# Kernel tuning notes

Hardware: AMD Instinct MI355X
Metric: run time of the kernel (lower is better)

The kernel has to match this reference:

```python
import jax, jax.numpy as jnp
import numpy as np

T, E, K, H, I = 512, 16, 4, 2880, 2880
G_H, G_I = H // 32, I // 32  # MXFP4 groups of 32 values (16 bytes/block)
ALPHA, LIMIT, EPS = 1.702, 7.0, 1e-5

FP4_VALUES = jnp.array([0.0, 0.5, 1.0, 1.5, 2.0, 3.0, 4.0, 6.0,
                        -0.0, -0.5, -1.0, -1.5, -2.0, -3.0, -4.0, -6.0], jnp.float32)


def dequant_mxfp4(blocks, scales):
    # blocks: uint8 [..., G, 16]; scales: uint8 [..., G] (biased exponent)
    pre = blocks.shape[:-2]
    G, B = blocks.shape[-2], blocks.shape[-1]
    lo = FP4_VALUES[(blocks & 0xF).astype(jnp.int32)]   # [..., G, B]
    hi = FP4_VALUES[(blocks >> 4).astype(jnp.int32)]    # [..., G, B]
    vals = jnp.stack([lo, hi], axis=-1).reshape(*pre, G, B * 2)  # interleave lo/hi per byte
    vals = jnp.ldexp(vals, (scales.astype(jnp.int32) - 127)[..., None])
    return vals.reshape(*pre, G * B * 2)


def swiglu(h):
    g = jnp.minimum(h[..., 0::2], LIMIT)
    l = jnp.clip(h[..., 1::2], -LIMIT, LIMIT)
    return g * jax.nn.sigmoid(ALPHA * g) * (l + 1.0)


def setup_inputs() -> dict:
    key = jax.random.key(0)
    ks = jax.random.split(key, 10)
    x = jax.random.normal(ks[0], (T, H), jnp.float32)
    norm_scale = jnp.ones((H,), jnp.float32)
    gate_w = jax.random.normal(ks[1], (E, H), jnp.float32) * 0.02
    gate_b = jnp.zeros((E,), jnp.float32)
    mlp1_blocks = jax.random.randint(ks[2], (E, 2 * I, G_H, 16), 0, 256, dtype=jnp.uint8)
    mlp1_scales = jax.random.randint(ks[3], (E, 2 * I, G_H), 118, 128, dtype=jnp.uint8)
    mlp1_bias = jax.random.normal(ks[4], (E, 2 * I), jnp.float32) * 0.02
    mlp2_blocks = jax.random.randint(ks[5], (E, H, G_I, 16), 0, 256, dtype=jnp.uint8)
    mlp2_scales = jax.random.randint(ks[6], (E, H, G_I), 118, 128, dtype=jnp.uint8)
    mlp2_bias = jax.random.normal(ks[7], (E, H), jnp.float32) * 0.02
    return {"x": x, "norm_scale": norm_scale, "gate_w": gate_w, "gate_b": gate_b,
            "mlp1_blocks": mlp1_blocks, "mlp1_scales": mlp1_scales, "mlp1_bias": mlp1_bias,
            "mlp2_blocks": mlp2_blocks, "mlp2_scales": mlp2_scales, "mlp2_bias": mlp2_bias}


def reference(x, norm_scale, gate_w, gate_b, mlp1_blocks, mlp1_scales, mlp1_bias,
              mlp2_blocks, mlp2_scales, mlp2_bias):
    # RMSNorm
    t = x * jax.lax.rsqrt(jnp.mean(x * x, axis=-1, keepdims=True) + EPS) * norm_scale
    # router: top-k + softmax over selected logits
    g = t @ gate_w.T + gate_b                      # [T, E]
    vals, idx = jax.lax.top_k(g, K)                # sorted, distinct indices
    w = jax.nn.softmax(vals, axis=-1)              # [T, K]
    n_tok = t.shape[0]
    route = jnp.zeros((n_tok, gate_w.shape[0]), t.dtype)
    route = route.at[jnp.arange(n_tok)[:, None], idx].set(w)  # [T, E] sparse weights
    # expert MLPs (dense dispatch; unrouted experts get zero weight)
    W1 = dequant_mxfp4(mlp1_blocks, mlp1_scales)   # [E, 2I, H]
    h = jnp.einsum('th,ech->tec', t, W1) + mlp1_bias[None]   # [T, E, 2I]
    h = swiglu(h)                                            # [T, E, I]
    W2 = dequant_mxfp4(mlp2_blocks, mlp2_scales)   # [E, H, I]
    o = jnp.einsum('tec,ehc->teh', h, W2) + mlp2_bias[None]  # [T, E, H]
    return x + jnp.einsum('teh,te->th', o, route)
```

## Files before the change

### kernel.cpp

```cpp
#include <hip/hip_runtime.h>
#include <hip/hip_bf16.h>

typedef __attribute__((ext_vector_type(8))) short short8;
typedef __attribute__((ext_vector_type(4))) float f32x4;
typedef __attribute__((ext_vector_type(4))) int i32x4;
typedef __attribute__((ext_vector_type(2))) int i32x2;
typedef __attribute__((ext_vector_type(4))) unsigned u32x4;

#define NTOK 512
#define NEXP 16
#define TOPK 4
#define HD   2880
#define ID   2880
#define N1   5760
#define NGRP 90
#define NKT  45
#define ROWB 5760

__device__ __forceinline__ unsigned perm(unsigned hi, unsigned lo, unsigned sel) {
  return __builtin_amdgcn_perm(hi, lo, sel);
}

__device__ __forceinline__ u32x4 dq_word4(unsigned p, unsigned hbl, unsigned hbh,
                                          unsigned lbl, unsigned lbh) {
  unsigned ph = p >> 4;
  unsigned il = p  & 0x07070707u, sl = p  & 0x08080808u;
  unsigned ih = ph & 0x07070707u, sh = ph & 0x08080808u;
  unsigned hbL = perm(hbh, hbl, il) | (sl << 4);
  unsigned lbL = perm(lbh, lbl, il);
  unsigned hbH = perm(hbh, hbl, ih) | (sh << 4);
  unsigned lbH = perm(lbh, lbl, ih);
  unsigned mL01 = perm(hbL, lbL, 0x05010400u);
  unsigned mL23 = perm(hbL, lbL, 0x07030602u);
  unsigned mH01 = perm(hbH, lbH, 0x05010400u);
  unsigned mH23 = perm(hbH, lbH, 0x07030602u);
  u32x4 w;
  w.x = perm(mH01, mL01, 0x05040100u);
  w.y = perm(mH01, mL01, 0x07060302u);
  w.z = perm(mH23, mL23, 0x05040100u);
  w.w = perm(mH23, mL23, 0x07060302u);
  return w;
}

__device__ __forceinline__ short8 dq_frag(i32x4 q, int sc) {
  unsigned m7 = (unsigned)((127 - sc) << 7);
  unsigned mm = m7 | (m7 << 16);
  unsigned e10 = (0x3F00u - m7) << 16;
  unsigned e32 = 0x3FC03F80u - mm;
  unsigned e54 = 0x40404000u - mm;
  unsigned e76 = 0x40C04080u - mm;
  unsigned hbl = perm(e32, e10, 0x07050301u);
  unsigned hbh = perm(e76, e54, 0x07050301u);
  unsigned lbl = perm(e32, e10, 0x06040200u);
  unsigned lbh = perm(e76, e54, 0x06040200u);
  unsigned pk = (unsigned)q.x | ((unsigned)q.y << 8) |
                ((unsigned)q.z << 16) | ((unsigned)q.w << 24);
  u32x4 w = dq_word4(pk, hbl, hbh, lbl, lbh);
  return __builtin_bit_cast(short8, w);
}

__global__ __launch_bounds__(256)
void rmsnorm_k(const float* __restrict__ x, const float* __restrict__ nsc,
               float* __restrict__ tf, __hip_bfloat16* __restrict__ tb,
               int* __restrict__ cnt)
{
  int t = blockIdx.x;
  if (t == 0 && threadIdx.x < NEXP) cnt[threadIdx.x] = 0;
  const float* xr = x + (size_t)t * HD;
  float s = 0.f;
  for (int i = threadIdx.x; i < HD; i += 256) { float v = xr[i]; s += v * v; }
#pragma unroll
  for (int o = 32; o > 0; o >>= 1) s += __shfl_down(s, o);
  __shared__ float red[4];
  if ((threadIdx.x & 63) == 0) red[threadIdx.x >> 6] = s;
  __syncthreads();
  float tot = red[0] + red[1] + red[2] + red[3];
  float rinv = rsqrtf(tot / (float)HD + 1e-5f);
  for (int i = threadIdx.x; i < HD; i += 256) {
    float v = xr[i] * rinv * nsc[i];
    tf[(size_t)t * HD + i] = v;
    tb[(size_t)t * HD + i] = __float2bfloat16(v);
  }
}

__global__ __launch_bounds__(256)
void router_k(const float* __restrict__ tf, const float* __restrict__ gw,
              const float* __restrict__ gb, float* __restrict__ wpair,
              int* __restrict__ cnt, int* __restrict__ tok_list, int* __restrict__ pair_list)
{
  int t = blockIdx.x;
  int tid = threadIdx.x;
  int e = tid >> 4, l16 = tid & 15;
  const float* tr = tf + (size_t)t * HD;
  float s = 0.f;
  for (int i = l16; i < HD; i += 16) s += tr[i] * gw[e * HD + i];
#pragma unroll
  for (int o = 1; o < 16; o <<= 1) s += __shfl_xor(s, o);
  __shared__ float logits[NEXP];
  if (l16 == 0) logits[e] = s + gb[e];
  __syncthreads();
  if (tid == 0) {
    float v[NEXP];
#pragma unroll
    for (int i = 0; i < NEXP; ++i) v[i] = logits[i];
    int idx[TOPK]; float val[TOPK];
#pragma unroll
    for (int k = 0; k < TOPK; ++k) {
      int bi = 0; float bv = -1e30f;
      for (int i = 0; i < NEXP; ++i) if (v[i] > bv) { bv = v[i]; bi = i; }
      idx[k] = bi; val[k] = bv; v[bi] = -1e30f;
    }
    float mx = val[0], sum = 0.f, w[TOPK];
#pragma unroll
    for (int k = 0; k < TOPK; ++k) { w[k] = __expf(val[k] - mx); sum += w[k]; }
#pragma unroll
    for (int k = 0; k < TOPK; ++k) {
      float wk = w[k] / sum;
      int ee = idx[k];
      int slot = atomicAdd(&cnt[ee], 1);
      tok_list[ee * NTOK + slot]  = t;
      pair_list[ee * NTOK + slot] = t * TOPK + k;
      wpair[t * TOPK + k] = wk;
    }
  }
}

#define SYNC_LGKM do { asm volatile("s_waitcnt lgkmcnt(0)" ::: "memory"); \
    __builtin_amdgcn_sched_barrier(0); __builtin_amdgcn_s_barrier(); \
    __builtin_amdgcn_sched_barrier(0); } while (0)
#define SYNC_PLAIN do { __builtin_amdgcn_sched_barrier(0); __builtin_amdgcn_s_barrier(); \
    __builtin_amdgcn_sched_barrier(0); } while (0)

template<int STAGE, int BN>
__global__ __launch_bounds__(256, 4)
void moe_gemm(const __hip_bfloat16* __restrict__ Asrc,
              const int* __restrict__ Bblk, const int* __restrict__ Bscl,
              const float* __restrict__ Bbias,
              const int* __restrict__ cnt,
              const int* __restrict__ tok_list, const int* __restrict__ pair_list,
              __hip_bfloat16* __restrict__ h_out, float* __restrict__ o_out)
{
  constexpr int NDIM = (STAGE == 1) ? N1 : HD;
  constexpr int NF   = BN / 64;
  const int e  = blockIdx.z;
  const int ne = cnt[e];
  const int m0 = blockIdx.y * 128;
  if (m0 >= ne) return;
  const int n0 = blockIdx.x * BN;
  const int tid = threadIdx.x;
  const int wave = tid >> 6, lane = tid & 63;
  const int l15 = lane & 15, l4 = lane >> 4;

  __shared__ __align__(16) char Abuf[2][16384];

  const int* glist = (STAGE == 1 ? tok_list : pair_list) + e * NTOK;
  const int* plist = pair_list + e * NTOK;

  const char* agp[4];
  int awoff[4];
#pragma unroll
  for (int c = 0; c < 4; ++c) {
    int g    = c * 256 + tid;
    int row  = g >> 3;
    int cb   = (g & 7) * 16;
    int slot = m0 + row; if (slot > ne - 1) slot = ne - 1;
    agp[c]   = (const char*)Asrc + (size_t)glist[slot] * ROWB + cb;
    awoff[c] = row * 128 + (cb ^ ((row & 7) << 4));
  }

  const int wn = wave * (16 * NF);
  unsigned bofs[NF], srow[NF];
#pragma unroll
  for (int f = 0; f < NF; ++f) {
    int row = n0 + wn + f * 16 + l15;
    unsigned rb = (unsigned)(e * NDIM + row) * NGRP;
    bofs[f] = rb * 16 + (unsigned)(l4 * 4);
    srow[f] = rb;
  }

  int aoff[8][2];
#pragma unroll
  for (int mf = 0; mf < 8; ++mf) {
    int row = mf * 16 + l15;
#pragma unroll
    for (int kk = 0; kk < 2; ++kk)
      aoff[mf][kk] = row * 128 + ((kk * 64 + l4 * 16) ^ ((row & 7) << 4));
  }

  f32x4 zero = {0.f, 0.f, 0.f, 0.f};
  f32x4 acc[8][NF];
#pragma unroll
  for (int a = 0; a < 8; ++a)
#pragma unroll
    for (int b = 0; b < NF; ++b) acc[a][b] = zero;

  i32x4 Ar[4];
  i32x4 q[NF][2]; i32x2 sc[NF];
  short8 b[NF][2];

#pragma unroll
  for (int c = 0; c < 4; ++c) Ar[c] = *(const i32x4*)agp[c];
#pragma unroll
  for (int f = 0; f < NF; ++f) {
    q[f][0] = *(const i32x4*)(Bblk + bofs[f]);
    q[f][1] = *(const i32x4*)(Bblk + bofs[f] + 16);
    sc[f]   = *(const i32x2*)(Bscl + srow[f]);
  }
#pragma unroll
  for (int c = 0; c < 4; ++c) *(i32x4*)(Abuf[0] + awoff[c]) = Ar[c];
#pragma unroll
  for (int f = 0; f < NF; ++f) {
    b[f][0] = dq_frag(q[f][0], sc[f].x);
    b[f][1] = dq_frag(q[f][1], sc[f].y);
  }
#pragma unroll
  for (int c = 0; c < 4; ++c) Ar[c] = *(const i32x4*)(agp[c] + 128);
#pragma unroll
  for (int f = 0; f < NF; ++f) {
    q[f][0] = *(const i32x4*)(Bblk + bofs[f] + 2 * 16);
    q[f][1] = *(const i32x4*)(Bblk + bofs[f] + 3 * 16);
    sc[f]   = *(const i32x2*)(Bscl + srow[f] + 2);
  }
  SYNC_LGKM;

  for (int t = 0; t < NKT; ++t) {
    const int cur = t & 1, nxt = cur ^ 1;
    int tld = t + 2; if (tld >= NKT) tld = NKT - 1;

#pragma unroll
    for (int c = 0; c < 4; ++c) *(i32x4*)(Abuf[nxt] + awoff[c]) = Ar[c];
#pragma unroll
    for (int c = 0; c < 4; ++c) Ar[c] = *(const i32x4*)(agp[c] + tld * 128);
    SYNC_LGKM;

    __builtin_amdgcn_s_setprio(1);
#pragma unroll
    for (int kk = 0; kk < 2; ++kk) {
#pragma unroll
      for (int mf = 0; mf < 8; ++mf) {
        short8 af = *(const short8*)(Abuf[cur] + aoff[mf][kk]);
#pragma unroll
        for (int nf = 0; nf < NF; ++nf)
          acc[mf][nf] = __builtin_amdgcn_mfma_f32_16x16x32_bf16(af, b[nf][kk], acc[mf][nf], 0, 0, 0);
      }
    }
    __builtin_amdgcn_s_setprio(0);

#pragma unroll
    for (int f = 0; f < NF; ++f) {
      b[f][0] = dq_frag(q[f][0], sc[f].x);
      b[f][1] = dq_frag(q[f][1], sc[f].y);
    }
#pragma unroll
    for (int f = 0; f < NF; ++f) {
      q[f][0] = *(const i32x4*)(Bblk + bofs[f] + (unsigned)((tld * 2 + 0) * 16));
      q[f][1] = *(const i32x4*)(Bblk + bofs[f] + (unsigned)((tld * 2 + 1) * 16));
      sc[f]   = *(const i32x2*)(Bscl + srow[f] + (unsigned)(tld * 2));
    }
    SYNC_PLAIN;
  }

  if (STAGE == 1) {
#pragma unroll
    for (int ma = 0; ma < 8; ++ma) {
#pragma unroll
      for (int nb = 0; nb < NF; ++nb) {
        int ncol = n0 + wn + nb * 16 + l15;
        float bias = Bbias[e * NDIM + ncol];
#pragma unroll
        for (int j = 0; j < 4; ++j) {
          float u  = acc[ma][nb][j] + bias;
          float up = __shfl_xor(u, 1);
          int slot = m0 + ma * 16 + l4 * 4 + j;
          if (!(lane & 1) && slot < ne) {
            float g  = fminf(u, 7.f);
            float lv = fminf(fmaxf(up, -7.f), 7.f);
            float hv = g / (1.f + __expf(-1.702f * g)) * (lv + 1.f);
            h_out[(size_t)plist[slot] * ID + (ncol >> 1)] = __float2bfloat16(hv);
          }
        }
      }
    }
  } else {
#pragma unroll
    for (int ma = 0; ma < 8; ++ma) {
#pragma unroll
      for (int nb = 0; nb < NF; ++nb) {
        int ncol = n0 + wn + nb * 16 + l15;
        float bias = Bbias[e * NDIM + ncol];
#pragma unroll
        for (int j = 0; j < 4; ++j) {
          int slot = m0 + ma * 16 + l4 * 4 + j;
          if (slot < ne)
            o_out[(size_t)plist[slot] * HD + ncol] = acc[ma][nb][j] + bias;
        }
      }
    }
  }
}

__global__ __launch_bounds__(256)
void final_k(const float* __restrict__ x, const float* __restrict__ obuf,
             const float* __restrict__ wpair, float* __restrict__ out)
{
  int t = blockIdx.x;
  float w0 = wpair[t * 4 + 0], w1 = wpair[t * 4 + 1];
  float w2 = wpair[t * 4 + 2], w3 = wpair[t * 4 + 3];
  const float* o0 = obuf + (size_t)(t * 4) * HD;
  for (int i = threadIdx.x; i < HD; i += 256) {
    float r = x[(size_t)t * HD + i]
            + w0 * o0[i] + w1 * o0[HD + i] + w2 * o0[2 * HD + i] + w3 * o0[3 * HD + i];
    out[(size_t)t * HD + i] = r;
  }
}

extern "C" void kernel_launch(void* const* d_in, const int* in_sizes, int n_in,
                              void* d_out, int out_size, void* d_ws, size_t ws_size,
                              hipStream_t stream)
{
  const float* x    = (const float*)d_in[0];
  const float* nsc  = (const float*)d_in[1];
  const float* gw   = (const float*)d_in[2];
  const float* gb   = (const float*)d_in[3];
  const int*   b1   = (const int*)d_in[4];
  const int*   s1   = (const int*)d_in[5];
  const float* bia1 = (const float*)d_in[6];
  const int*   b2   = (const int*)d_in[7];
  const int*   s2   = (const int*)d_in[8];
  const float* bia2 = (const float*)d_in[9];
  float* out = (float*)d_out;

  char* ws = (char*)d_ws;
  size_t off = 0;
  auto alloc = [&](size_t bytes) {
    char* p = ws + off;
    off = (off + bytes + 255) & ~(size_t)255;
    return p;
  };
  float*           tf    = (float*)alloc((size_t)NTOK * HD * 4);
  __hip_bfloat16*  tb    = (__hip_bfloat16*)alloc((size_t)NTOK * HD * 2);
  __hip_bfloat16*  hbuf  = (__hip_bfloat16*)alloc((size_t)NTOK * TOPK * ID * 2);
  float*           obuf  = (float*)alloc((size_t)NTOK * TOPK * HD * 4);
  float*           wpair = (float*)alloc(NTOK * TOPK * 4);
  int*             cnt   = (int*)alloc(64);
  int*             tokl  = (int*)alloc(NEXP * NTOK * 4);
  int*             pairl = (int*)alloc(NEXP * NTOK * 4);

  rmsnorm_k<<<NTOK, 256, 0, stream>>>(x, nsc, tf, tb, cnt);
  router_k<<<NTOK, 256, 0, stream>>>(tf, gw, gb, wpair, cnt, tokl, pairl);
  moe_gemm<1, 64><<<dim3(N1 / 64, 4, NEXP), 256, 0, stream>>>(tb, b1, s1, bia1, cnt, tokl, pairl, hbuf, nullptr);
  moe_gemm<2, 64><<<dim3(HD / 64, 4, NEXP), 256, 0, stream>>>(hbuf, b2, s2, bia2, cnt, tokl, pairl, nullptr, obuf);
  final_k<<<NTOK, 256, 0, stream>>>(x, obuf, wpair, out);
}
```

Before: 467.6 us.

## Repack int32-per-byte MXFP4 weights and scales into compact bytes before GEMMs

Adds a pack kernel that squeezes the int32-per-byte weight blocks and scales into dense uint8 buffers in workspace on every call. The MoE GEMMs then read 4-byte words instead of 16-byte vectors per fragment, which cuts the bytes the GEMM streams from memory. It also removes the in-kernel byte packing and drops the BN template parameter in favor of a fixed single fragment. The cost is an extra full read of the int32 weights plus a write of the packed copy each call, and a fallback path when the workspace is too small.

```diff
diff --git a/kernel.cpp b/kernel.cpp
--- a/kernel.cpp
+++ b/kernel.cpp
@@ -16,6 +16,11 @@
 #define NGRP 90
 #define NKT  45
 #define ROWB 5760
+
+#define NB1 132710400
+#define NS1 8294400
+#define NB2 66355200
+#define NS2 4147200
 
 __device__ __forceinline__ unsigned perm(unsigned hi, unsigned lo, unsigned sel) {
   return __builtin_amdgcn_perm(hi, lo, sel);
@@ -42,7 +47,7 @@
   return w;
 }
 
-__device__ __forceinline__ short8 dq_frag(i32x4 q, int sc) {
+__device__ __forceinline__ short8 dq_frag(unsigned pk, int sc) {
   unsigned m7 = (unsigned)((127 - sc) << 7);
   unsigned mm = m7 | (m7 << 16);
   unsigned e10 = (0x3F00u - m7) << 16;
@@ -53,10 +58,27 @@
   unsigned hbh = perm(e76, e54, 0x07050301u);
   unsigned lbl = perm(e32, e10, 0x06040200u);
   unsigned lbh = perm(e76, e54, 0x06040200u);
-  unsigned pk = (unsigned)q.x | ((unsigned)q.y << 8) |
-                ((unsigned)q.z << 16) | ((unsigned)q.w << 24);
   u32x4 w = dq_word4(pk, hbl, hbh, lbl, lbh);
   return __builtin_bit_cast(short8, w);
+}
+
+__global__ __launch_bounds__(256)
+void pack_k(const int* __restrict__ in, unsigned char* __restrict__ out, int n16)
+{
+  int i = blockIdx.x * 256 + threadIdx.x;
+  if (i >= n16) return;
+  const i32x4* p = (const i32x4*)(in + (size_t)i * 16);
+  i32x4 a = p[0], b = p[1], c = p[2], d = p[3];
+  u32x4 w;
+  w.x = (unsigned)(a.x & 255) | ((unsigned)(a.y & 255) << 8) |
+        ((unsigned)(a.z & 255) << 16) | ((unsigned)a.w << 24);
+  w.y = (unsigned)(b.x & 255) | ((unsigned)(b.y & 255) << 8) |
+        ((unsigned)(b.z & 255) << 16) | ((unsigned)b.w << 24);
+  w.z = (unsigned)(c.x & 255) | ((unsigned)(c.y & 255) << 8) |
+        ((unsigned)(c.z & 255) << 16) | ((unsigned)c.w << 24);
+  w.w = (unsigned)(d.x & 255) | ((unsigned)(d.y & 255) << 8) |
+        ((unsigned)(d.z & 255) << 16) | ((unsigned)d.w << 24);
+  *(u32x4*)(out + (size_t)i * 16) = w;
 }
 
 __global__ __launch_bounds__(256)
@@ -131,22 +153,22 @@
 #define SYNC_PLAIN do { __builtin_amdgcn_sched_barrier(0); __builtin_amdgcn_s_barrier(); \
     __builtin_amdgcn_sched_barrier(0); } while (0)
 
-template<int STAGE, int BN>
+template<int STAGE, bool PACKED>
 __global__ __launch_bounds__(256, 4)
 void moe_gemm(const __hip_bfloat16* __restrict__ Asrc,
-              const int* __restrict__ Bblk, const int* __restrict__ Bscl,
+              const void* __restrict__ Bblk_, const void* __restrict__ Bscl_,
               const float* __restrict__ Bbias,
               const int* __restrict__ cnt,
               const int* __restrict__ tok_list, const int* __restrict__ pair_list,
               __hip_bfloat16* __restrict__ h_out, float* __restrict__ o_out)
 {
   constexpr int NDIM = (STAGE == 1) ? N1 : HD;
-  constexpr int NF   = BN / 64;
+  constexpr int NF   = 1;
   const int e  = blockIdx.z;
   const int ne = cnt[e];
   const int m0 = blockIdx.y * 128;
   if (m0 >= ne) return;
-  const int n0 = blockIdx.x * BN;
+  const int n0 = blockIdx.x * 64;
   const int tid = threadIdx.x;
   const int wave = tid >> 6, lane = tid & 63;
   const int l15 = lane & 15, l4 = lane >> 4;
@@ -168,15 +190,21 @@
     awoff[c] = row * 128 + (cb ^ ((row & 7) << 4));
   }
 
-  const int wn = wave * (16 * NF);
-  unsigned bofs[NF], srow[NF];
-#pragma unroll
-  for (int f = 0; f < NF; ++f) {
-    int row = n0 + wn + f * 16 + l15;
-    unsigned rb = (unsigned)(e * NDIM + row) * NGRP;
-    bofs[f] = rb * 16 + (unsigned)(l4 * 4);
-    srow[f] = rb;
-  }
+  const int wn = wave * 16;
+  const int brow = n0 + wn + l15;
+  unsigned bofs, srow;
+  if (PACKED) {
+    bofs = (unsigned)(e * NDIM + brow) * (NGRP * 16u) + (unsigned)(l4 * 4);
+    srow = (unsigned)(e * NDIM + brow) * (unsigned)NGRP;
+  } else {
+    unsigned rb = (unsigned)(e * NDIM + brow) * NGRP;
+    bofs = rb * 16 + (unsigned)(l4 * 4);
+    srow = rb;
+  }
+  const unsigned char* Bp = (const unsigned char*)Bblk_;
+  const unsigned char* Sp = (const unsigned char*)Bscl_;
+  const int* Bw = (const int*)Bblk_;
+  const int* Sw = (const int*)Bscl_;
 
   int aoff[8][2];
 #pragma unroll
@@ -190,37 +218,41 @@
   f32x4 zero = {0.f, 0.f, 0.f, 0.f};
   f32x4 acc[8][NF];
 #pragma unroll
-  for (int a = 0; a < 8; ++a)
-#pragma unroll
-    for (int b = 0; b < NF; ++b) acc[a][b] = zero;
+  for (int a = 0; a < 8; ++a) acc[a][0] = zero;
 
   i32x4 Ar[4];
-  i32x4 q[NF][2]; i32x2 sc[NF];
-  short8 b[NF][2];
+  unsigned q0, q1;
+  int scx, scy;
+  short8 b0, b1;
+
+  auto loadB = [&](int tt) {
+    if (PACKED) {
+      q0 = *(const unsigned*)(Bp + bofs + (unsigned)(tt * 32));
+      q1 = *(const unsigned*)(Bp + bofs + (unsigned)(tt * 32 + 16));
+      unsigned sv = *(const unsigned short*)(Sp + srow + (unsigned)(tt * 2));
+      scx = (int)(sv & 255u); scy = (int)(sv >> 8);
+    } else {
+      i32x4 v0 = *(const i32x4*)(Bw + bofs + (unsigned)((tt * 2 + 0) * 16));
+      i32x4 v1 = *(const i32x4*)(Bw + bofs + (unsigned)((tt * 2 + 1) * 16));
+      q0 = (unsigned)(v0.x & 255) | ((unsigned)(v0.y & 255) << 8) |
+           ((unsigned)(v0.z & 255) << 16) | ((unsigned)v0.w << 24);
+      q1 = (unsigned)(v1.x & 255) | ((unsigned)(v1.y & 255) << 8) |
+           ((unsigned)(v1.z & 255) << 16) | ((unsigned)v1.w << 24);
+      i32x2 sv = *(const i32x2*)(Sw + srow + (unsigned)(tt * 2));
+      scx = sv.x; scy = sv.y;
+    }
+  };
 
 #pragma unroll
   for (int c = 0; c < 4; ++c) Ar[c] = *(const i32x4*)agp[c];
-#pragma unroll
-  for (int f = 0; f < NF; ++f) {
-    q[f][0] = *(const i32x4*)(Bblk + bofs[f]);
-    q[f][1] = *(const i32x4*)(Bblk + bofs[f] + 16);
-    sc[f]   = *(const i32x2*)(Bscl + srow[f]);
-  }
+  loadB(0);
 #pragma unroll
   for (int c = 0; c < 4; ++c) *(i32x4*)(Abuf[0] + awoff[c]) = Ar[c];
-#pragma unroll
-  for (int f = 0; f < NF; ++f) {
-    b[f][0] = dq_frag(q[f][0], sc[f].x);
-    b[f][1] = dq_frag(q[f][1], sc[f].y);
-  }
+  b0 = dq_frag(q0, scx);
+  b1 = dq_frag(q1, scy);
 #pragma unroll
   for (int c = 0; c < 4; ++c) Ar[c] = *(const i32x4*)(agp[c] + 128);
-#pragma unroll
-  for (int f = 0; f < NF; ++f) {
-    q[f][0] = *(const i32x4*)(Bblk + bofs[f] + 2 * 16);
-    q[f][1] = *(const i32x4*)(Bblk + bofs[f] + 3 * 16);
-    sc[f]   = *(const i32x2*)(Bscl + srow[f] + 2);
-  }
+  loadB(1);
   SYNC_LGKM;
 
   for (int t = 0; t < NKT; ++t) {
@@ -236,64 +268,49 @@
     __builtin_amdgcn_s_setprio(1);
 #pragma unroll
     for (int kk = 0; kk < 2; ++kk) {
+      short8 bk = kk ? b1 : b0;
 #pragma unroll
       for (int mf = 0; mf < 8; ++mf) {
         short8 af = *(const short8*)(Abuf[cur] + aoff[mf][kk]);
-#pragma unroll
-        for (int nf = 0; nf < NF; ++nf)
-          acc[mf][nf] = __builtin_amdgcn_mfma_f32_16x16x32_bf16(af, b[nf][kk], acc[mf][nf], 0, 0, 0);
+        acc[mf][0] = __builtin_amdgcn_mfma_f32_16x16x32_bf16(af, bk, acc[mf][0], 0, 0, 0);
       }
     }
     __builtin_amdgcn_s_setprio(0);
 
-#pragma unroll
-    for (int f = 0; f < NF; ++f) {
-      b[f][0] = dq_frag(q[f][0], sc[f].x);
-      b[f][1] = dq_frag(q[f][1], sc[f].y);
-    }
-#pragma unroll
-    for (int f = 0; f < NF; ++f) {
-      q[f][0] = *(const i32x4*)(Bblk + bofs[f] + (unsigned)((tld * 2 + 0) * 16));
-      q[f][1] = *(const i32x4*)(Bblk + bofs[f] + (unsigned)((tld * 2 + 1) * 16));
-      sc[f]   = *(const i32x2*)(Bscl + srow[f] + (unsigned)(tld * 2));
-    }
+    b0 = dq_frag(q0, scx);
+    b1 = dq_frag(q1, scy);
+    loadB(tld);
     SYNC_PLAIN;
   }
 
   if (STAGE == 1) {
 #pragma unroll
     for (int ma = 0; ma < 8; ++ma) {
-#pragma unroll
-      for (int nb = 0; nb < NF; ++nb) {
-        int ncol = n0 + wn + nb * 16 + l15;
-        float bias = Bbias[e * NDIM + ncol];
-#pragma unroll
-        for (int j = 0; j < 4; ++j) {
-          float u  = acc[ma][nb][j] + bias;
-          float up = __shfl_xor(u, 1);
-          int slot = m0 + ma * 16 + l4 * 4 + j;
-          if (!(lane & 1) && slot < ne) {
-            float g  = fminf(u, 7.f);
-            float lv = fminf(fmaxf(up, -7.f), 7.f);
-            float hv = g / (1.f + __expf(-1.702f * g)) * (lv + 1.f);
-            h_out[(size_t)plist[slot] * ID + (ncol >> 1)] = __float2bfloat16(hv);
-          }
+      int ncol = n0 + wn + l15;
+      float bias = Bbias[e * NDIM + ncol];
+#pragma unroll
+      for (int j = 0; j < 4; ++j) {
+        float u  = acc[ma][0][j] + bias;
+        float up = __shfl_xor(u, 1);
+        int slot = m0 + ma * 16 + l4 * 4 + j;
+        if (!(lane & 1) && slot < ne) {
+          float g  = fminf(u, 7.f);
+          float lv = fminf(fmaxf(up, -7.f), 7.f);
+          float hv = g / (1.f + __expf(-1.702f * g)) * (lv + 1.f);
+          h_out[(size_t)plist[slot] * ID + (ncol >> 1)] = __float2bfloat16(hv);
         }
       }
     }
   } else {
 #pragma unroll
     for (int ma = 0; ma < 8; ++ma) {
-#pragma unroll
-      for (int nb = 0; nb < NF; ++nb) {
-        int ncol = n0 + wn + nb * 16 + l15;
-        float bias = Bbias[e * NDIM + ncol];
-#pragma unroll
-        for (int j = 0; j < 4; ++j) {
-          int slot = m0 + ma * 16 + l4 * 4 + j;
-          if (slot < ne)
-            o_out[(size_t)plist[slot] * HD + ncol] = acc[ma][nb][j] + bias;
-        }
+      int ncol = n0 + wn + l15;
+      float bias = Bbias[e * NDIM + ncol];
+#pragma unroll
+      for (int j = 0; j < 4; ++j) {
+        int slot = m0 + ma * 16 + l4 * 4 + j;
+        if (slot < ne)
+          o_out[(size_t)plist[slot] * HD + ncol] = acc[ma][0][j] + bias;
       }
     }
   }
@@ -345,10 +362,28 @@
   int*             cnt   = (int*)alloc(64);
   int*             tokl  = (int*)alloc(NEXP * NTOK * 4);
   int*             pairl = (int*)alloc(NEXP * NTOK * 4);
+  unsigned char*   pb1   = (unsigned char*)alloc(NB1);
+  unsigned char*   ps1   = (unsigned char*)alloc(NS1);
+  unsigned char*   pb2   = (unsigned char*)alloc(NB2);
+  unsigned char*   ps2   = (unsigned char*)alloc(NS2);
+  const bool packed = (off <= ws_size);
 
   rmsnorm_k<<<NTOK, 256, 0, stream>>>(x, nsc, tf, tb, cnt);
   router_k<<<NTOK, 256, 0, stream>>>(tf, gw, gb, wpair, cnt, tokl, pairl);
-  moe_gemm<1, 64><<<dim3(N1 / 64, 4, NEXP), 256, 0, stream>>>(tb, b1, s1, bia1, cnt, tokl, pairl, hbuf, nullptr);
-  moe_gemm<2, 64><<<dim3(HD / 64, 4, NEXP), 256, 0, stream>>>(hbuf, b2, s2, bia2, cnt, tokl, pairl, nullptr, obuf);
+  if (packed) {
+    pack_k<<<(NB1 / 16 + 255) / 256, 256, 0, stream>>>(b1, pb1, NB1 / 16);
+    pack_k<<<(NS1 / 16 + 255) / 256, 256, 0, stream>>>(s1, ps1, NS1 / 16);
+    pack_k<<<(NB2 / 16 + 255) / 256, 256, 0, stream>>>(b2, pb2, NB2 / 16);
+    pack_k<<<(NS2 / 16 + 255) / 256, 256, 0, stream>>>(s2, ps2, NS2 / 16);
+    moe_gemm<1, true><<<dim3(N1 / 64, 4, NEXP), 256, 0, stream>>>(
+        tb, pb1, ps1, bia1, cnt, tokl, pairl, hbuf, nullptr);
+    moe_gemm<2, true><<<dim3(HD / 64, 4, NEXP), 256, 0, stream>>>(
+        hbuf, pb2, ps2, bia2, cnt, tokl, pairl, nullptr, obuf);
+  } else {
+    moe_gemm<1, false><<<dim3(N1 / 64, 4, NEXP), 256, 0, stream>>>(
+        tb, b1, s1, bia1, cnt, tokl, pairl, hbuf, nullptr);
+    moe_gemm<2, false><<<dim3(HD / 64, 4, NEXP), 256, 0, stream>>>(
+        hbuf, b2, s2, bia2, cnt, tokl, pairl, nullptr, obuf);
+  }
   final_k<<<NTOK, 256, 0, stream>>>(x, obuf, wpair, out);
 }
```

New measurement: 599.5 us. +28.2%, slower.
